# Performance work log

Measured on AMD Instinct MI355X. Metric: run time of the kernel, lower is better.

## Reference

```python
import jax, jax.numpy as jnp
import numpy as np

L, B, P, D, H, DH, KV, M, S, A = 12, 8, 800, 1024, 8, 256, 1, 4096, 50, 32
ROPE_BASE = 10000.0
NEG = -1e30


def _rms(x, w):
    return (x * jax.lax.rsqrt(jnp.mean(x * x, -1, keepdims=True) + 1e-6)) * (1.0 + w)


def _rope(x, cos, sin):
    # x: [B,h,S,DH]; cos/sin: [B,1,S,DH//2]
    x1, x2 = jnp.split(x, 2, axis=-1)
    return jnp.concatenate([x1 * cos - x2 * sin, x2 * cos + x1 * sin], -1)


def setup_inputs() -> dict:
    key = jax.random.key(0)
    ks = iter(jax.random.split(key, 40))
    def nrm(shape, s=0.02):
        return jax.random.normal(next(ks), shape, jnp.float32) * s
    return {
        'prefix_pad_masks': jnp.ones((B, P), jnp.bool_),
        'x_t': jax.random.normal(next(ks), (B, S, A), jnp.float32),
        'timestep': jax.random.uniform(next(ks), (B,), jnp.float32),
        'dt': jnp.full((1,), 0.1, jnp.float32),
        'cache_k': nrm((L, B, KV, P, DH), 1.0),
        'cache_v': nrm((L, B, KV, P, DH), 1.0),
        'w_act_in': nrm((A, D)), 'b_act_in': jnp.zeros((D,), jnp.float32),
        'w_t1': nrm((D, D)), 'b_t1': jnp.zeros((D,), jnp.float32),
        'w_t2': nrm((D, D)), 'b_t2': jnp.zeros((D,), jnp.float32),
        'ln1_w': jnp.zeros((L, D), jnp.float32),
        'ada1_w': nrm((L, D, D)),
        'ln2_w': jnp.zeros((L, D), jnp.float32),
        'wq': nrm((L, D, H * DH)), 'wk': nrm((L, D, KV * DH)),
        'wv': nrm((L, D, KV * DH)), 'wo': nrm((L, H * DH, D)),
        'wg': nrm((L, D, M)), 'wu': nrm((L, D, M)), 'wd': nrm((L, M, D)),
        'lnf_w': jnp.zeros((D,), jnp.float32), 'adaf_w': nrm((D, D)),
        'w_act_out': nrm((D, A)), 'b_act_out': jnp.zeros((A,), jnp.float32),
    }


def reference(prefix_pad_masks, x_t, timestep, dt, cache_k, cache_v,
              w_act_in, b_act_in, w_t1, b_t1, w_t2, b_t2,
              ln1_w, ada1_w, ln2_w, wq, wk, wv, wo, wg, wu, wd,
              lnf_w, adaf_w, w_act_out, b_act_out):
    b, s, _ = x_t.shape
    p = prefix_pad_masks.shape[1]
    # --- embed_suffix: action projection + sinusoidal time -> MLP -> adaRMS cond ---
    suffix = x_t @ w_act_in + b_act_in                              # [B,S,D]
    half = D // 2
    freqs = jnp.exp(-jnp.log(jnp.float32(10000.0)) * jnp.arange(half, dtype=jnp.float32) / half)
    ang = timestep[:, None] * freqs[None, :]
    temb = jnp.concatenate([jnp.sin(ang), jnp.cos(ang)], -1)        # [B,D]
    cond = jax.nn.silu(temb @ w_t1 + b_t1) @ w_t2 + b_t2            # adarms_cond [B,D]
    # --- prefix-suffix 2D attention mask (make_att_2d_masks_trt) ---
    suffix_pad = jnp.ones((b, s), jnp.int32)
    suffix_att = jnp.concatenate([jnp.ones((b, 1), jnp.int32), jnp.zeros((b, s - 1), jnp.int32)], 1)
    cums = jnp.cumsum(suffix_att, 1)
    att2d = cums[:, None, :] <= cums[:, :, None]
    pad2d = (suffix_pad[:, None, :] * suffix_pad[:, :, None]).astype(bool)
    pre2d = jnp.broadcast_to(prefix_pad_masks[:, None, :], (b, s, p))
    full = jnp.concatenate([pre2d, att2d & pad2d], 2)               # [B,S,P+S]
    bias = jnp.where(full, 0.0, NEG)[:, None, :, :].astype(jnp.float32)
    # --- position ids: prefix offset + suffix cumsum - 1 ---
    offs = jnp.sum(prefix_pad_masks.astype(jnp.int32), -1)[:, None]
    pos = offs + jnp.cumsum(suffix_pad, 1) - 1                      # [B,S]
    inv = 1.0 / (ROPE_BASE ** (jnp.arange(0, DH, 2, dtype=jnp.float32) / DH))
    rang = pos[..., None].astype(jnp.float32) * inv                 # [B,S,DH/2]
    cos = jnp.cos(rang)[:, None]
    sin = jnp.sin(rang)[:, None]
    # --- gemma expert (eager attention over KV cache + suffix) ---
    h = suffix * jnp.sqrt(jnp.float32(D))
    def layer(hc, xs):
        l1, a1, l2, Wq, Wk, Wv, Wo, Wg, Wu, Wd, ck, cv = xs
        x = _rms(hc, l1) * (1.0 + (cond @ a1)[:, None, :])
        q = (x @ Wq).reshape(b, s, H, DH).transpose(0, 2, 1, 3)
        k = (x @ Wk).reshape(b, s, KV, DH).transpose(0, 2, 1, 3)
        v = (x @ Wv).reshape(b, s, KV, DH).transpose(0, 2, 1, 3)
        q = _rope(q, cos, sin)
        k = _rope(k, cos, sin)
        kf = jnp.repeat(jnp.concatenate([ck, k], 2), H // KV, 1)    # [B,H,P+S,DH]
        vf = jnp.repeat(jnp.concatenate([cv, v], 2), H // KV, 1)
        sc = jnp.einsum('bhsd,bhtd->bhst', q, kf) / jnp.sqrt(jnp.float32(DH)) + bias
        at = jax.nn.softmax(sc, -1)
        o = jnp.einsum('bhst,bhtd->bhsd', at, vf).transpose(0, 2, 1, 3).reshape(b, s, H * DH)
        hc = hc + o @ Wo
        x2 = _rms(hc, l2)
        hc = hc + (jax.nn.gelu(x2 @ Wg, approximate=True) * (x2 @ Wu)) @ Wd
        return hc, None
    h, _ = jax.lax.scan(layer, h, (ln1_w, ada1_w, ln2_w, wq, wk, wv, wo, wg, wu, wd, cache_k, cache_v))
    hf = _rms(h, lnf_w) * (1.0 + (cond @ adaf_w)[:, None, :])
    v_t = hf[:, -S:].astype(jnp.float32) @ w_act_out + b_act_out    # action_out_proj
    return x_t + dt.reshape(1, 1, 1) * v_t                          # Euler step
```

## Files before the change

### kernel.cpp

```cpp
#include <hip/hip_runtime.h>
#include <hip/hip_bf16.h>
#include <math.h>

#define NLAYER 12
#define NB 8
#define NP 800
#define ND 1024
#define NH 8
#define NDH 256
#define NM 4096
#define NS 50
#define NA 32
#define NKEYS 850
#define KPAD 896

typedef unsigned short ushort_t;
typedef unsigned int u32;
using f32x4  = __attribute__((ext_vector_type(4))) float;
using short8 = __attribute__((ext_vector_type(8))) short;

__device__ __forceinline__ u32 pack_bf2(float lo, float hi) {
  u32 a = __float_as_uint(lo);
  u32 b = __float_as_uint(hi);
  a += 0x7fffu + ((a >> 16) & 1u);
  b += 0x7fffu + ((b >> 16) & 1u);
  return (a >> 16) | (b & 0xffff0000u);
}
__device__ __forceinline__ ushort_t bf1(float x) {
  u32 a = __float_as_uint(x);
  a += 0x7fffu + ((a >> 16) & 1u);
  return (ushort_t)(a >> 16);
}
__device__ __forceinline__ float ubf(ushort_t h) {
  return __uint_as_float(((u32)h) << 16);
}
__device__ __forceinline__ void async_cp16(const void* g, const void* l) {
  __builtin_amdgcn_global_load_lds(
      (const __attribute__((address_space(1))) u32*)g,
      (__attribute__((address_space(3))) u32*)l, 16, 0, 0);
}


__global__ void cvt_copy_kernel(const float* __restrict__ src, ushort_t* __restrict__ dst, long n) {
  long i = ((long)blockIdx.x * 256 + threadIdx.x) * 8;
  if (i >= n) return;
  const float4* s4 = reinterpret_cast<const float4*>(src + i);
  float4 a = s4[0], b = s4[1];
  *reinterpret_cast<uint4*>(dst + i) =
      make_uint4(pack_bf2(a.x, a.y), pack_bf2(a.z, a.w),
                 pack_bf2(b.x, b.y), pack_bf2(b.z, b.w));
}

template<int MODE>
__global__ __launch_bounds__(256) void transpose_cvt(
    const float* __restrict__ src, long sz, ushort_t* __restrict__ dst, long dz,
    int R, int C, int ldd, int halfOff) {
  __shared__ float Ls[64][65];
  const float* s = src + (long)blockIdx.z * sz;
  ushort_t* d    = dst + (long)blockIdx.z * dz;
  int c0 = blockIdx.x * 64, r0 = blockIdx.y * 64;
  int t = threadIdx.x;
  int rr = t >> 4;
  int cc = (t & 15) * 4;
#pragma unroll
  for (int j = 0; j < 4; ++j) {
    int rl = rr + j * 16;
    int r = r0 + rl;
    float4 v = make_float4(0.f, 0.f, 0.f, 0.f);
    if (r < R) v = *reinterpret_cast<const float4*>(s + (long)r * C + c0 + cc);
    Ls[rl][cc] = v.x; Ls[rl][cc+1] = v.y; Ls[rl][cc+2] = v.z; Ls[rl][cc+3] = v.w;
  }
  __syncthreads();
  int dr = t >> 2;
  int rc = (t & 3) * 16;
  int cg = c0 + dr;
  long orow;
  if (MODE == 0) orow = cg;
  else           orow = ((long)(cg >> 5) << 6) + (cg & 31) + halfOff;
  ushort_t* drow = d + orow * ldd + r0 + rc;
#pragma unroll
  for (int i = 0; i < 16; i += 2) {
    int sr = r0 + rc + i;
    if (sr < R) {
      u32 p = pack_bf2(Ls[rc + i][dr], Ls[rc + i + 1][dr]);
      *reinterpret_cast<u32*>(drow + i) = p;
    }
  }
}


__global__ void temb_kernel(const float* __restrict__ ts, float* __restrict__ temb) {
  int idx = blockIdx.x * 256 + threadIdx.x;
  if (idx >= NB * ND) return;
  int b = idx >> 10, d = idx & 1023;
  int i = d & 511;
  float f = __expf(-logf(10000.f) * (float)i / 512.f);
  float ang = ts[b] * f;
  temb[idx] = (d < 512) ? sinf(ang) : cosf(ang);
}

__global__ void suffix_kernel(const float* __restrict__ x_t, const float* __restrict__ w,
                              const float* __restrict__ bias, float* __restrict__ h) {
  int m = blockIdx.x;
  __shared__ float xs[NA];
  if (threadIdx.x < NA) xs[threadIdx.x] = x_t[m * NA + threadIdx.x];
  __syncthreads();
  for (int n = threadIdx.x; n < ND; n += 256) {
    float acc = bias[n];
#pragma unroll
    for (int k = 0; k < NA; ++k) acc += xs[k] * w[k * ND + n];
    h[m * ND + n] = acc * 32.0f;
  }
}

__global__ void rope_table_kernel(float* __restrict__ cosT, float* __restrict__ sinT) {
  int idx = blockIdx.x * 256 + threadIdx.x;
  if (idx >= NS * 128) return;
  int s = idx >> 7, i = idx & 127;
  float inv = __expf(-(float)(2 * i) / 256.f * logf(10000.f));
  float ang = (float)(NP + s) * inv;
  cosT[idx] = cosf(ang);
  sinT[idx] = sinf(ang);
}

__global__ void rope3_kernel(const ushort_t* __restrict__ qkv0, const ushort_t* __restrict__ qkv1,
                             const float* __restrict__ cosT, const float* __restrict__ sinT,
                             ushort_t* __restrict__ qT, ushort_t* __restrict__ k_new,
                             ushort_t* __restrict__ vT_l) {
  int idx = blockIdx.x * 256 + threadIdx.x;
  if (idx >= 400 * 10 * 128) return;
  int i = idx & 127;
  int rest = idx >> 7;
  int hh = rest % 10;
  int m = rest / 10;
  int b = m / NS, s = m % NS;
  if (hh == 9) {
    int d = i;
    long base = (long)m * 2560 + 2304;
    float v0 = ubf(qkv0[base + d])       + ubf(qkv1[base + d]);
    float v1 = ubf(qkv0[base + d + 128]) + ubf(qkv1[base + d + 128]);
    vT_l[((long)(b * 256 + d)) * KPAD + NP + s]       = bf1(v0);
    vT_l[((long)(b * 256 + d + 128)) * KPAD + NP + s] = bf1(v1);
    return;
  }
  float c = cosT[s * 128 + i], sn = sinT[s * 128 + i];
  if (hh < NH) {
    long base = (long)m * 2560 + hh * 256;
    float x1 = ubf(qkv0[base + i])       + ubf(qkv1[base + i]);
    float x2 = ubf(qkv0[base + 128 + i]) + ubf(qkv1[base + 128 + i]);
    ushort_t* dst = qT + (((long)(b * NH + hh) * NS + s) * 256);
    dst[i]       = bf1(x1 * c - x2 * sn);
    dst[128 + i] = bf1(x2 * c + x1 * sn);
  } else {
    long base = (long)m * 2560 + 2048;
    float x1 = ubf(qkv0[base + i])       + ubf(qkv1[base + i]);
    float x2 = ubf(qkv0[base + 128 + i]) + ubf(qkv1[base + 128 + i]);
    ushort_t* dst = k_new + (long)m * 256;
    dst[i]       = bf1(x1 * c - x2 * sn);
    dst[128 + i] = bf1(x2 * c + x1 * sn);
  }
}

template<bool BFOUT>
__global__ void rms_kernel(const float* __restrict__ hin, const float* __restrict__ w,
                           const float* __restrict__ ada, void* __restrict__ outv) {
  int m = blockIdx.x;
  int b = m / NS;
  int d0 = threadIdx.x * 4;
  float4 v = *reinterpret_cast<const float4*>(hin + (long)m * ND + d0);
  float ss = v.x*v.x + v.y*v.y + v.z*v.z + v.w*v.w;
#pragma unroll
  for (int off = 32; off > 0; off >>= 1) ss += __shfl_down(ss, off);
  __shared__ float red[4];
  int lane = threadIdx.x & 63, wid = threadIdx.x >> 6;
  if (lane == 0) red[wid] = ss;
  __syncthreads();
  float tot = red[0] + red[1] + red[2] + red[3];
  float r = rsqrtf(tot * (1.f / ND) + 1e-6f);
  float4 wv = *reinterpret_cast<const float4*>(w + d0);
  float4 o;
  o.x = v.x * r * (1.f + wv.x);
  o.y = v.y * r * (1.f + wv.y);
  o.z = v.z * r * (1.f + wv.z);
  o.w = v.w * r * (1.f + wv.w);
  if (ada) {
    float4 av = *reinterpret_cast<const float4*>(ada + (long)b * ND + d0);
    o.x *= (1.f + av.x); o.y *= (1.f + av.y); o.z *= (1.f + av.z); o.w *= (1.f + av.w);
  }
  if (BFOUT) {
    *reinterpret_cast<uint2*>((ushort_t*)outv + (long)m * ND + d0) =
        make_uint2(pack_bf2(o.x, o.y), pack_bf2(o.z, o.w));
  } else {
    *reinterpret_cast<float4*>((float*)outv + (long)m * ND + d0) = o;
  }
}

__global__ void softmax_kernel(const float* __restrict__ sc, ushort_t* __restrict__ P) {
  int row = blockIdx.x;
  const float* p = sc + (long)row * KPAD;
  ushort_t* o = P + (long)row * KPAD;
  __shared__ float e[NKEYS];
  __shared__ float red[4];
  int lane = threadIdx.x & 63, wid = threadIdx.x >> 6;
  float mx = -1e30f;
  for (int t = threadIdx.x; t < NKEYS; t += 256) { float v = p[t]; e[t] = v; mx = fmaxf(mx, v); }
#pragma unroll
  for (int off = 32; off > 0; off >>= 1) mx = fmaxf(mx, __shfl_down(mx, off));
  if (lane == 0) red[wid] = mx;
  __syncthreads();
  mx = fmaxf(fmaxf(red[0], red[1]), fmaxf(red[2], red[3]));
  __syncthreads();
  float sum = 0.f;
  for (int t = threadIdx.x; t < NKEYS; t += 256) {
    float v = __expf(e[t] - mx);
    e[t] = v;
    sum += v;
  }
#pragma unroll
  for (int off = 32; off > 0; off >>= 1) sum += __shfl_down(sum, off);
  if (lane == 0) red[wid] = sum;
  __syncthreads();
  float inv = 1.f / (red[0] + red[1] + red[2] + red[3]);
  for (int t = threadIdx.x; t < KPAD; t += 256)
    o[t] = (t < NKEYS) ? bf1(e[t] * inv) : (ushort_t)0;
}

__global__ void final_kernel(const float* __restrict__ hf, const float* __restrict__ w,
                             const float* __restrict__ bias, const float* __restrict__ x_t,
                             const float* __restrict__ dt, float* __restrict__ out) {
  int m = blockIdx.x;
  int a = threadIdx.x & 31;
  int kg = threadIdx.x >> 5;
  float acc = 0.f;
  for (int k = kg; k < ND; k += 8) acc += hf[(long)m * ND + k] * w[k * NA + a];
  __shared__ float red[256];
  red[threadIdx.x] = acc;
  __syncthreads();
  if (threadIdx.x < NA) {
    float s = 0.f;
#pragma unroll
    for (int g = 0; g < 8; ++g) s += red[g * 32 + a];
    out[m * NA + a] = x_t[m * NA + a] + dt[0] * (s + bias[a]);
  }
}

template<int EPI, bool SPL, bool SPLITK>
__global__ __launch_bounds__(256) void gemm64(
    const ushort_t* __restrict__ A, long az,
    const ushort_t* __restrict__ B1, long b1z,
    const ushort_t* __restrict__ B2, long b2z, int nsplit, int nlim2,
    void* __restrict__ Cv, long cz,
    int M, int N, int K, int lda, int ldb, int ldc,
    float scale, int kpb, const ushort_t* __restrict__ zpad) {
  int z = blockIdx.z;
  int chunk = 0;
  int kbeg = 0, kend = K;
  if (SPLITK) { chunk = z; kbeg = z * kpb; kend = kbeg + kpb; z = 0; }
  const ushort_t* Ab  = A  + (long)z * az;
  const ushort_t* B1b = B1 + (long)z * b1z;
  const ushort_t* B2b = SPL ? (B2 + (long)z * b2z) : nullptr;

  const int m0 = blockIdx.x * 64;
  const int n0 = blockIdx.y * 64;
  const int tid = threadIdx.x;
  const int lane = tid & 63;
  const int wbase = tid & 192;
  const int wid = wbase >> 6;
  const int wm = (wid >> 1) * 32;
  const int wn = (wid & 1) * 32;
  const int l15 = lane & 15;
  const int l4  = lane >> 4;

  __shared__ ushort_t As[2][64 * 64];
  __shared__ ushort_t Bs[2][64 * 64];

  f32x4 acc[2][2] = {};

  const int ci0 = wbase + lane;
  const int row0 = ci0 >> 3;
  const int kc0 = (ci0 & 7) << 3;
  const int ci1 = 256 + ci0;
  const int row1 = ci1 >> 3;
  const int kc1 = (ci1 & 7) << 3;
  int gra0 = m0 + row0; if (gra0 > M - 1) gra0 = M - 1;
  int gra1 = m0 + row1; if (gra1 > M - 1) gra1 = M - 1;
  const int n_0 = n0 + row0;
  const int n_1 = n0 + row1;

  auto stage = [&](int buf, int k0) {
    async_cp16(Ab + (long)gra0 * lda + k0 + kc0, (const char*)As[buf] + (wbase + lane) * 16 - lane * 16 + lane * 16);
    const ushort_t* gp0;
    const ushort_t* gp1;
    if (SPL) {
      gp0 = (n_0 < nsplit) ? B1b + (long)n_0 * ldb + k0 + kc0
          : (n_0 < nlim2)  ? B2b + (long)(n_0 - nsplit) * ldb + k0 + kc0
                           : zpad + kc0;
      gp1 = (n_1 < nsplit) ? B1b + (long)n_1 * ldb + k0 + kc1
          : (n_1 < nlim2)  ? B2b + (long)(n_1 - nsplit) * ldb + k0 + kc1
                           : zpad + kc1;
    } else {
      gp0 = B1b + (long)n_0 * ldb + k0 + kc0;
      gp1 = B1b + (long)n_1 * ldb + k0 + kc1;
    }
    async_cp16(gp0, (const char*)Bs[buf] + ci0 * 16);
    async_cp16(Ab + (long)gra1 * lda + k0 + kc1, (const char*)As[buf] + ci1 * 16);
    async_cp16(gp1, (const char*)Bs[buf] + ci1 * 16);
  };

  const int nt = (kend - kbeg) >> 6;
  stage(0, kbeg);
  __syncthreads();
  int cur = 0;
  for (int t = 0; t < nt; ++t) {
    if (t + 1 < nt) stage(cur ^ 1, kbeg + (t + 1) * 64);
    const ushort_t* Ac = As[cur];
    const ushort_t* Bc = Bs[cur];
#pragma unroll
    for (int ks = 0; ks < 2; ++ks) {
      short8 af[2], bf[2];
#pragma unroll
      for (int mi = 0; mi < 2; ++mi)
        af[mi] = *reinterpret_cast<const short8*>(&Ac[(wm + mi * 16 + l15) * 64 + ks * 32 + l4 * 8]);
#pragma unroll
      for (int ni = 0; ni < 2; ++ni)
        bf[ni] = *reinterpret_cast<const short8*>(&Bc[(wn + ni * 16 + l15) * 64 + ks * 32 + l4 * 8]);
#pragma unroll
      for (int mi = 0; mi < 2; ++mi)
#pragma unroll
        for (int ni = 0; ni < 2; ++ni)
          acc[mi][ni] = __builtin_amdgcn_mfma_f32_16x16x32_bf16(af[mi], bf[ni], acc[mi][ni], 0, 0, 0);
    }
    __syncthreads();
    cur ^= 1;
  }

#pragma unroll
  for (int mi = 0; mi < 2; ++mi) {
#pragma unroll
    for (int ni = 0; ni < 2; ++ni) {
      int col = n0 + wn + ni * 16 + l15;
      int rb  = m0 + wm + mi * 16 + l4 * 4;
      if (col >= N) continue;
#pragma unroll
      for (int r = 0; r < 4; ++r) {
        int row = rb + r;
        if (row >= M) continue;
        float v = acc[mi][ni][r];
        if (EPI == 0) {
          ((float*)Cv)[(long)z * cz + (long)row * ldc + col] = v * scale;
        } else if (EPI == 3) {
          atomicAdd(&((float*)Cv)[(long)row * ldc + col], v);
        } else if (EPI == 4) {
          int hh = row / NS;
          int s  = row - hh * NS;
          ((ushort_t*)Cv)[((long)(blockIdx.z * NS + s)) * 2048 + hh * 256 + col] = bf1(v);
        } else if (EPI == 5) {
          long slab = SPLITK ? (long)chunk : (long)z;
          ((ushort_t*)Cv)[slab * cz + (long)row * ldc + col] = bf1(v);
        }
      }
    }
  }
}

__global__ __launch_bounds__(256) void gemm64G(
    const ushort_t* __restrict__ A, const ushort_t* __restrict__ B,
    ushort_t* __restrict__ C, int M, int K, int lda, int ldb, int ldc) {
  const int m0 = blockIdx.x * 64;
  const int n0 = blockIdx.y * 64;
  const int tid = threadIdx.x;
  const int lane = tid & 63;
  const int wbase = tid & 192;
  const int wid = wbase >> 6;
  const int l15 = lane & 15;
  const int l4  = lane >> 4;

  __shared__ ushort_t As[2][64 * 64];
  __shared__ ushort_t Bs[2][64 * 64];

  f32x4 acc[4] = {};

  const int ci0 = wbase + lane;
  const int row0 = ci0 >> 3;
  const int kc0 = (ci0 & 7) << 3;
  const int ci1 = 256 + ci0;
  const int row1 = ci1 >> 3;
  const int kc1 = (ci1 & 7) << 3;
  int gra0 = m0 + row0; if (gra0 > M - 1) gra0 = M - 1;
  int gra1 = m0 + row1; if (gra1 > M - 1) gra1 = M - 1;

  auto stage = [&](int buf, int k0) {
    async_cp16(A + (long)gra0 * lda + k0 + kc0, (const char*)As[buf] + ci0 * 16);
    async_cp16(B + (long)(n0 + row0) * ldb + k0 + kc0, (const char*)Bs[buf] + ci0 * 16);
    async_cp16(A + (long)gra1 * lda + k0 + kc1, (const char*)As[buf] + ci1 * 16);
    async_cp16(B + (long)(n0 + row1) * ldb + k0 + kc1, (const char*)Bs[buf] + ci1 * 16);
  };

  const int nt = K >> 6;
  stage(0, 0);
  __syncthreads();
  int cur = 0;
  for (int t = 0; t < nt; ++t) {
    if (t + 1 < nt) stage(cur ^ 1, (t + 1) * 64);
    const ushort_t* Ac = As[cur];
    const ushort_t* Bc = Bs[cur];
#pragma unroll
    for (int ks = 0; ks < 2; ++ks) {
      short8 af = *reinterpret_cast<const short8*>(&Ac[(wid * 16 + l15) * 64 + ks * 32 + l4 * 8]);
#pragma unroll
      for (int ni = 0; ni < 4; ++ni) {
        short8 bf = *reinterpret_cast<const short8*>(&Bc[(ni * 16 + l15) * 64 + ks * 32 + l4 * 8]);
        acc[ni] = __builtin_amdgcn_mfma_f32_16x16x32_bf16(af, bf, acc[ni], 0, 0, 0);
      }
    }
    __syncthreads();
    cur ^= 1;
  }

#pragma unroll
  for (int ni = 0; ni < 2; ++ni) {
    int col = (n0 >> 1) + ni * 16 + l15;
    int rb  = m0 + wid * 16 + l4 * 4;
#pragma unroll
    for (int r = 0; r < 4; ++r) {
      int row = rb + r;
      if (row >= M) continue;
      float g = acc[ni][r];
      float u = acc[ni + 2][r];
      float inner = 0.7978845608028654f * (g + 0.044715f * g * g * g);
      float t = 0.5f * g * (1.f + tanhf(inner));
      C[(long)row * ldc + col] = bf1(t * u);
    }
  }
}

template<int EPI>
__global__ __launch_bounds__(256)
void gemm_f32_kernel(const float* __restrict__ A,
                     const float* __restrict__ B1,
                     float* __restrict__ C,
                     int M, int N, int K, int lda, int ldb, int ldc,
                     const float* __restrict__ bias) {
  const int m0 = blockIdx.x * 64;
  const int n0 = blockIdx.y * 64;
  const int tid = threadIdx.x;
  const int lane = tid & 63;
  const int wid = tid >> 6;
  const int wm = (wid >> 1) * 32;
  const int wn = (wid & 1) * 32;
  const int l15 = lane & 15;
  const int l4  = lane >> 4;

  __shared__ __align__(16) ushort_t As[64][72];
  __shared__ __align__(16) ushort_t Bs[64][72];

  f32x4 acc[2][2] = {};

  for (int k0 = 0; k0 < K; k0 += 64) {
#pragma unroll
    for (int pass = 0; pass < 2; ++pass) {
      int c = tid + pass * 256;
      int row = c >> 3;
      int kc = (c & 7) * 8;
      int gr = m0 + row, gk = k0 + kc;
      float v[8];
#pragma unroll
      for (int j = 0; j < 8; ++j)
        v[j] = (gr < M && gk + j < K) ? A[(long)gr * lda + gk + j] : 0.f;
      *reinterpret_cast<uint4*>(&As[row][kc]) =
          make_uint4(pack_bf2(v[0],v[1]), pack_bf2(v[2],v[3]),
                     pack_bf2(v[4],v[5]), pack_bf2(v[6],v[7]));
    }
    {
      int n = tid & 63;
      int kg = tid >> 6;
      int gn = n0 + n;
      u32 pk[8];
#pragma unroll
      for (int kk = 0; kk < 16; kk += 2) {
        int kga = k0 + kg * 16 + kk;
        float v0 = (gn < N && kga < K)     ? B1[(long)kga * ldb + gn] : 0.f;
        float v1 = (gn < N && kga + 1 < K) ? B1[(long)(kga + 1) * ldb + gn] : 0.f;
        pk[kk >> 1] = pack_bf2(v0, v1);
      }
      *reinterpret_cast<uint4*>(&Bs[n][kg * 16])     = make_uint4(pk[0],pk[1],pk[2],pk[3]);
      *reinterpret_cast<uint4*>(&Bs[n][kg * 16 + 8]) = make_uint4(pk[4],pk[5],pk[6],pk[7]);
    }
    __syncthreads();
#pragma unroll
    for (int ks = 0; ks < 2; ++ks) {
      short8 af[2], bfr[2];
#pragma unroll
      for (int mi = 0; mi < 2; ++mi)
        af[mi] = *reinterpret_cast<const short8*>(&As[wm + mi*16 + l15][ks*32 + l4*8]);
#pragma unroll
      for (int ni = 0; ni < 2; ++ni)
        bfr[ni] = *reinterpret_cast<const short8*>(&Bs[wn + ni*16 + l15][ks*32 + l4*8]);
#pragma unroll
      for (int mi = 0; mi < 2; ++mi)
#pragma unroll
        for (int ni = 0; ni < 2; ++ni)
          acc[mi][ni] = __builtin_amdgcn_mfma_f32_16x16x32_bf16(af[mi], bfr[ni], acc[mi][ni], 0, 0, 0);
    }
    __syncthreads();
  }

#pragma unroll
  for (int mi = 0; mi < 2; ++mi) {
#pragma unroll
    for (int ni = 0; ni < 2; ++ni) {
      int col = n0 + wn + ni * 16 + l15;
      int rb  = m0 + wm + mi * 16 + l4 * 4;
#pragma unroll
      for (int r = 0; r < 4; ++r) {
        int row = rb + r;
        if (row < M && col < N) {
          float v = acc[mi][ni][r];
          if (EPI == 1) C[(long)row * ldc + col] = v + bias[col];
          else {
            float t = v + bias[col];
            C[(long)row * ldc + col] = t / (1.f + __expf(-t));
          }
        }
      }
    }
  }
}

__global__ __launch_bounds__(256)
void gemm_f32sk(const float* __restrict__ A,
                const float* __restrict__ B, long bz,
                float* __restrict__ C, long cz,
                int M, int N, int K, int lda, int ldb, int ldc, int nks) {
  const int zz = blockIdx.z;
  const int layer = zz / nks;
  const int chunk = zz % nks;
  const int kpb = K / nks;
  const int kbeg = chunk * kpb, kend = kbeg + kpb;
  const float* Bb = B + (long)layer * bz;
  float* Cb = C + (long)layer * cz;

  const int m0 = blockIdx.x * 64;
  const int n0 = blockIdx.y * 64;
  const int tid = threadIdx.x;
  const int lane = tid & 63;
  const int wid = tid >> 6;
  const int wm = (wid >> 1) * 32;
  const int wn = (wid & 1) * 32;
  const int l15 = lane & 15;
  const int l4  = lane >> 4;

  __shared__ __align__(16) ushort_t As[64][72];
  __shared__ __align__(16) ushort_t Bs[64][72];

  f32x4 acc[2][2] = {};

  for (int k0 = kbeg; k0 < kend; k0 += 64) {
#pragma unroll
    for (int pass = 0; pass < 2; ++pass) {
      int c = tid + pass * 256;
      int row = c >> 3;
      int kc = (c & 7) * 8;
      int gr = m0 + row, gk = k0 + kc;
      float v[8];
#pragma unroll
      for (int j = 0; j < 8; ++j)
        v[j] = (gr < M) ? A[(long)gr * lda + gk + j] : 0.f;
      *reinterpret_cast<uint4*>(&As[row][kc]) =
          make_uint4(pack_bf2(v[0],v[1]), pack_bf2(v[2],v[3]),
                     pack_bf2(v[4],v[5]), pack_bf2(v[6],v[7]));
    }
    {
      int n = tid & 63;
      int kg = tid >> 6;
      int gn = n0 + n;
      u32 pk[8];
#pragma unroll
      for (int kk = 0; kk < 16; kk += 2) {
        int kga = k0 + kg * 16 + kk;
        float v0 = Bb[(long)kga * ldb + gn];
        float v1 = Bb[(long)(kga + 1) * ldb + gn];
        pk[kk >> 1] = pack_bf2(v0, v1);
      }
      *reinterpret_cast<uint4*>(&Bs[n][kg * 16])     = make_uint4(pk[0],pk[1],pk[2],pk[3]);
      *reinterpret_cast<uint4*>(&Bs[n][kg * 16 + 8]) = make_uint4(pk[4],pk[5],pk[6],pk[7]);
    }
    __syncthreads();
#pragma unroll
    for (int ks = 0; ks < 2; ++ks) {
      short8 af[2], bfr[2];
#pragma unroll
      for (int mi = 0; mi < 2; ++mi)
        af[mi] = *reinterpret_cast<const short8*>(&As[wm + mi*16 + l15][ks*32 + l4*8]);
#pragma unroll
      for (int ni = 0; ni < 2; ++ni)
        bfr[ni] = *reinterpret_cast<const short8*>(&Bs[wn + ni*16 + l15][ks*32 + l4*8]);
#pragma unroll
      for (int mi = 0; mi < 2; ++mi)
#pragma unroll
        for (int ni = 0; ni < 2; ++ni)
          acc[mi][ni] = __builtin_amdgcn_mfma_f32_16x16x32_bf16(af[mi], bfr[ni], acc[mi][ni], 0, 0, 0);
    }
    __syncthreads();
  }

#pragma unroll
  for (int mi = 0; mi < 2; ++mi) {
#pragma unroll
    for (int ni = 0; ni < 2; ++ni) {
      int col = n0 + wn + ni * 16 + l15;
      int rb  = m0 + wm + mi * 16 + l4 * 4;
#pragma unroll
      for (int r = 0; r < 4; ++r) {
        int row = rb + r;
        if (row < M && col < N)
          atomicAdd(&Cb[(long)row * ldc + col], acc[mi][ni][r]);
      }
    }
  }
}

extern "C" void kernel_launch(void* const* d_in, const int* in_sizes, int n_in,
                              void* d_out, int out_size, void* d_ws, size_t ws_size,
                              hipStream_t stream) {
  (void)in_sizes; (void)n_in; (void)out_size; (void)ws_size;
  const float* x_t      = (const float*)d_in[1];
  const float* tstep    = (const float*)d_in[2];
  const float* dtp      = (const float*)d_in[3];
  const float* cache_k  = (const float*)d_in[4];
  const float* cache_v  = (const float*)d_in[5];
  const float* w_act_in = (const float*)d_in[6];
  const float* b_act_in = (const float*)d_in[7];
  const float* w_t1     = (const float*)d_in[8];
  const float* b_t1     = (const float*)d_in[9];
  const float* w_t2     = (const float*)d_in[10];
  const float* b_t2     = (const float*)d_in[11];
  const float* ln1_w    = (const float*)d_in[12];
  const float* ada1_w   = (const float*)d_in[13];
  const float* ln2_w    = (const float*)d_in[14];
  const float* wq       = (const float*)d_in[15];
  const float* wk       = (const float*)d_in[16];
  const float* wv       = (const float*)d_in[17];
  const float* wo       = (const float*)d_in[18];
  const float* wg       = (const float*)d_in[19];
  const float* wu       = (const float*)d_in[20];
  const float* wd       = (const float*)d_in[21];
  const float* lnf_w    = (const float*)d_in[22];
  const float* adaf_w   = (const float*)d_in[23];
  const float* wao      = (const float*)d_in[24];
  const float* bao      = (const float*)d_in[25];
  float* outp = (float*)d_out;

  char* p = (char*)d_ws;
  auto alloc = [&](size_t bytes) { char* r = p; p += (bytes + 255) & ~(size_t)255; return r; };

  ushort_t* wqkvT  = (ushort_t*)alloc((size_t)12 * 2560 * 1024 * 2);
  ushort_t* woT    = (ushort_t*)alloc((size_t)12 * 1024 * 2048 * 2);
  ushort_t* wguT   = (ushort_t*)alloc((size_t)12 * 8192 * 1024 * 2);
  ushort_t* wdT    = (ushort_t*)alloc((size_t)12 * 1024 * 4096 * 2);
  ushort_t* kcache = (ushort_t*)alloc((size_t)12 * 8 * NP * 256 * 2);
  ushort_t* vT     = (ushort_t*)alloc((size_t)12 * 8 * 256 * KPAD * 2);
  ushort_t* qkvp   = (ushort_t*)alloc((size_t)2 * 400 * 2560 * 2);
  ushort_t* qT     = (ushort_t*)alloc((size_t)8 * 400 * 256 * 2);
  ushort_t* k_new  = (ushort_t*)alloc((size_t)400 * 256 * 2);
  float*    sc     = (float*)alloc((size_t)8 * 400 * KPAD * 4);
  ushort_t* P      = (ushort_t*)alloc((size_t)8 * 400 * KPAD * 2);
  ushort_t* o_buf  = (ushort_t*)alloc((size_t)400 * 2048 * 2);
  ushort_t* t_buf  = (ushort_t*)alloc((size_t)400 * 4096 * 2);
  ushort_t* x_buf  = (ushort_t*)alloc((size_t)400 * 1024 * 2);
  float*    h_buf  = (float*)alloc((size_t)400 * 1024 * 4);
  float*    hf     = (float*)alloc((size_t)400 * 1024 * 4);
  float*    temb   = (float*)alloc(8 * 1024 * 4);
  float*    tmp    = (float*)alloc(8 * 1024 * 4);
  float*    cond   = (float*)alloc(8 * 1024 * 4);
  float*    ada_all= (float*)alloc((size_t)12 * 8 * 1024 * 4);
  float*    adaf_o = (float*)alloc(8 * 1024 * 4);
  float*    cosT   = (float*)alloc(NS * 128 * 4);
  float*    sinT   = (float*)alloc(NS * 128 * 4);
  ushort_t* zpad   = (ushort_t*)alloc(512 * 2);

  hipMemsetAsync(zpad, 0, 512 * 2, stream);
  hipMemsetAsync(ada_all, 0, ((size_t)12 * 8 * 1024 + 8 * 1024) * 4, stream);

  {
    long n = (long)12 * 8 * NP * 256;
    cvt_copy_kernel<<<(int)((n / 8 + 255) / 256), 256, 0, stream>>>(cache_k, kcache, n);
  }
  transpose_cvt<0><<<dim3(32, 16, 12), 256, 0, stream>>>(wq, (long)1024 * 2048, wqkvT, (long)2560 * 1024, 1024, 2048, 1024, 0);
  transpose_cvt<0><<<dim3(4, 16, 12), 256, 0, stream>>>(wk, (long)1024 * 256, wqkvT + (long)2048 * 1024, (long)2560 * 1024, 1024, 256, 1024, 0);
  transpose_cvt<0><<<dim3(4, 16, 12), 256, 0, stream>>>(wv, (long)1024 * 256, wqkvT + (long)2304 * 1024, (long)2560 * 1024, 1024, 256, 1024, 0);
  transpose_cvt<0><<<dim3(16, 32, 12), 256, 0, stream>>>(wo, (long)2048 * 1024, woT, (long)1024 * 2048, 2048, 1024, 2048, 0);
  transpose_cvt<1><<<dim3(64, 16, 12), 256, 0, stream>>>(wg, (long)1024 * 4096, wguT, (long)8192 * 1024, 1024, 4096, 1024, 0);
  transpose_cvt<1><<<dim3(64, 16, 12), 256, 0, stream>>>(wu, (long)1024 * 4096, wguT, (long)8192 * 1024, 1024, 4096, 1024, 32);
  transpose_cvt<0><<<dim3(16, 64, 12), 256, 0, stream>>>(wd, (long)4096 * 1024, wdT, (long)1024 * 4096, 4096, 1024, 4096, 0);
  transpose_cvt<0><<<dim3(4, 13, 96), 256, 0, stream>>>(cache_v, (long)NP * 256, vT, (long)256 * KPAD, NP, 256, KPAD, 0);

  temb_kernel<<<32, 256, 0, stream>>>(tstep, temb);
  suffix_kernel<<<400, 256, 0, stream>>>(x_t, w_act_in, b_act_in, h_buf);
  rope_table_kernel<<<25, 256, 0, stream>>>(cosT, sinT);
  gemm_f32_kernel<2><<<dim3(1, 16, 1), 256, 0, stream>>>(temb, w_t1, tmp, NB, ND, ND, ND, ND, ND, b_t1);
  gemm_f32_kernel<1><<<dim3(1, 16, 1), 256, 0, stream>>>(tmp, w_t2, cond, NB, ND, ND, ND, ND, ND, b_t2);
  gemm_f32sk<<<dim3(1, 16, 48), 256, 0, stream>>>(cond, ada1_w, (long)ND * ND, ada_all, (long)NB * ND, NB, ND, ND, ND, ND, ND, 4);
  gemm_f32sk<<<dim3(1, 16, 4), 256, 0, stream>>>(cond, adaf_w, 0, adaf_o, 0, NB, ND, ND, ND, ND, ND, 4);

  for (int l = 0; l < NLAYER; ++l) {
    rms_kernel<true><<<400, 256, 0, stream>>>(h_buf, ln1_w + (long)l * ND, ada_all + (long)l * NB * ND, x_buf);
    gemm64<5, false, true><<<dim3(7, 40, 2), 256, 0, stream>>>(
        x_buf, 0, wqkvT + (long)l * 2560 * 1024, 0, nullptr, 0, 0, 0,
        qkvp, (long)400 * 2560, 400, 2560, 1024, 1024, 1024, 2560, 1.f, 512, zpad);
    rope3_kernel<<<2000, 256, 0, stream>>>(qkvp, qkvp + (long)400 * 2560, cosT, sinT,
                                           qT, k_new, vT + (long)l * 8 * 256 * KPAD);
    gemm64<0, true, false><<<dim3(7, 14, 8), 256, 0, stream>>>(
        qT, (long)400 * 256,
        kcache + (long)l * 8 * NP * 256, (long)NP * 256,
        k_new, (long)NS * 256, NP, NKEYS,
        sc, (long)400 * KPAD, 400, KPAD, 256, 256, 256, KPAD, 0.0625f, 0, zpad);
    softmax_kernel<<<3200, 256, 0, stream>>>(sc, P);
    gemm64<4, false, false><<<dim3(7, 4, 8), 256, 0, stream>>>(
        P, (long)400 * KPAD,
        vT + (long)l * 8 * 256 * KPAD, (long)256 * KPAD, nullptr, 0, 0, 0,
        o_buf, 0, 400, 256, KPAD, KPAD, KPAD, 2048, 1.f, 0, zpad);
    gemm64<3, false, true><<<dim3(7, 16, 4), 256, 0, stream>>>(
        o_buf, 0, woT + (long)l * 1024 * 2048, 0, nullptr, 0, 0, 0,
        h_buf, 0, 400, 1024, 2048, 2048, 2048, 1024, 1.f, 512, zpad);
    rms_kernel<true><<<400, 256, 0, stream>>>(h_buf, ln2_w + (long)l * ND, nullptr, x_buf);
    gemm64G<<<dim3(7, 128, 1), 256, 0, stream>>>(
        x_buf, wguT + (long)l * 8192 * 1024, t_buf, 400, 1024, 1024, 1024, 4096);
    gemm64<3, false, true><<<dim3(7, 16, 4), 256, 0, stream>>>(
        t_buf, 0, wdT + (long)l * 1024 * 4096, 0, nullptr, 0, 0, 0,
        h_buf, 0, 400, 1024, 4096, 4096, 4096, 1024, 1.f, 1024, zpad);
  }

  rms_kernel<false><<<400, 256, 0, stream>>>(h_buf, lnf_w, adaf_o, hf);
  final_kernel<<<400, 256, 0, stream>>>(hf, wao, bao, x_t, dtp, outp);
}
```

Measured before the change: 2.049 ms.

## Use 128x128 block tiles for QKV, gate-up, and down projections

Adds a 128x128-tile MFMA GEMM kernel in which each wave computes a 64x64 sub-tile, and uses it for the QKV projection, the fused gate/up GELU projection and the down projection, replacing the 64x64 kernels. Larger tiles raise operand reuse from shared memory and global memory for each MFMA, which cuts load traffic. The cost is fewer blocks (for example 4x20x2 and 4x8x8), more LDS and registers per block, and lower occupancy. The down projection also moves to 8-way split-K with atomic adds, which doubles the atomic traffic into h_buf. With M=400, the last row tile of 128 is mostly padding.

```diff
diff --git a/kernel.cpp b/kernel.cpp
--- a/kernel.cpp
+++ b/kernel.cpp
@@ -288,7 +288,7 @@
   const int n_1 = n0 + row1;
 
   auto stage = [&](int buf, int k0) {
-    async_cp16(Ab + (long)gra0 * lda + k0 + kc0, (const char*)As[buf] + (wbase + lane) * 16 - lane * 16 + lane * 16);
+    async_cp16(Ab + (long)gra0 * lda + k0 + kc0, (const char*)As[buf] + ci0 * 16);
     const ushort_t* gp0;
     const ushort_t* gp1;
     if (SPL) {
@@ -363,37 +363,135 @@
   }
 }
 
-__global__ __launch_bounds__(256) void gemm64G(
+template<int EPI, bool SPLITK>
+__global__ __launch_bounds__(256) void gemm128(
+    const ushort_t* __restrict__ A,
+    const ushort_t* __restrict__ B,
+    void* __restrict__ Cv, long cz,
+    int M, int K, int lda, int ldb, int ldc, int kpb) {
+  const int chunk = SPLITK ? blockIdx.z : 0;
+  const int kbeg = SPLITK ? chunk * kpb : 0;
+  const int kend = SPLITK ? kbeg + kpb : K;
+
+  const int m0 = blockIdx.x * 128;
+  const int n0 = blockIdx.y * 128;
+  const int tid = threadIdx.x;
+  const int lane = tid & 63;
+  const int wid = tid >> 6;
+  const int wm = (wid >> 1) * 64;
+  const int wn = (wid & 1) * 64;
+  const int l15 = lane & 15;
+  const int l4  = lane >> 4;
+
+  __shared__ ushort_t As[2][128 * 64];
+  __shared__ ushort_t Bs[2][128 * 64];
+
+  f32x4 acc[4][4] = {};
+
+  int arow[4], brow[4], kcs[4];
+#pragma unroll
+  for (int i = 0; i < 4; ++i) {
+    int ci = i * 256 + tid;
+    int row = ci >> 3;
+    kcs[i] = (ci & 7) << 3;
+    int gr = m0 + row; if (gr > M - 1) gr = M - 1;
+    arow[i] = gr;
+    brow[i] = n0 + row;
+  }
+
+  auto stage = [&](int buf, int k0) {
+#pragma unroll
+    for (int i = 0; i < 4; ++i) {
+      int ci = i * 256 + tid;
+      async_cp16(A + (long)arow[i] * lda + k0 + kcs[i], (const char*)As[buf] + ci * 16);
+      async_cp16(B + (long)brow[i] * ldb + k0 + kcs[i], (const char*)Bs[buf] + ci * 16);
+    }
+  };
+
+  const int nt = (kend - kbeg) >> 6;
+  stage(0, kbeg);
+  __syncthreads();
+  int cur = 0;
+  for (int t = 0; t < nt; ++t) {
+    if (t + 1 < nt) stage(cur ^ 1, kbeg + (t + 1) * 64);
+    const ushort_t* Ac = As[cur];
+    const ushort_t* Bc = Bs[cur];
+#pragma unroll
+    for (int ks = 0; ks < 2; ++ks) {
+      short8 af[4], bf[4];
+#pragma unroll
+      for (int mi = 0; mi < 4; ++mi)
+        af[mi] = *reinterpret_cast<const short8*>(&Ac[(wm + mi * 16 + l15) * 64 + ks * 32 + l4 * 8]);
+#pragma unroll
+      for (int ni = 0; ni < 4; ++ni)
+        bf[ni] = *reinterpret_cast<const short8*>(&Bc[(wn + ni * 16 + l15) * 64 + ks * 32 + l4 * 8]);
+#pragma unroll
+      for (int mi = 0; mi < 4; ++mi)
+#pragma unroll
+        for (int ni = 0; ni < 4; ++ni)
+          acc[mi][ni] = __builtin_amdgcn_mfma_f32_16x16x32_bf16(af[mi], bf[ni], acc[mi][ni], 0, 0, 0);
+    }
+    __syncthreads();
+    cur ^= 1;
+  }
+
+#pragma unroll
+  for (int mi = 0; mi < 4; ++mi) {
+#pragma unroll
+    for (int ni = 0; ni < 4; ++ni) {
+      int col = n0 + wn + ni * 16 + l15;
+      int rb  = m0 + wm + mi * 16 + l4 * 4;
+#pragma unroll
+      for (int r = 0; r < 4; ++r) {
+        int row = rb + r;
+        if (row >= M) continue;
+        float v = acc[mi][ni][r];
+        if (EPI == 3) {
+          atomicAdd(&((float*)Cv)[(long)row * ldc + col], v);
+        } else {
+          ((ushort_t*)Cv)[(long)chunk * cz + (long)row * ldc + col] = bf1(v);
+        }
+      }
+    }
+  }
+}
+
+__global__ __launch_bounds__(256) void gemm128G(
     const ushort_t* __restrict__ A, const ushort_t* __restrict__ B,
     ushort_t* __restrict__ C, int M, int K, int lda, int ldb, int ldc) {
-  const int m0 = blockIdx.x * 64;
-  const int n0 = blockIdx.y * 64;
+  const int m0 = blockIdx.x * 128;
+  const int n0 = blockIdx.y * 128;
   const int tid = threadIdx.x;
   const int lane = tid & 63;
-  const int wbase = tid & 192;
-  const int wid = wbase >> 6;
+  const int wid = tid >> 6;
+  const int wm = (wid >> 1) * 64;
+  const int wn = (wid & 1) * 64;
   const int l15 = lane & 15;
   const int l4  = lane >> 4;
 
-  __shared__ ushort_t As[2][64 * 64];
-  __shared__ ushort_t Bs[2][64 * 64];
-
-  f32x4 acc[4] = {};
-
-  const int ci0 = wbase + lane;
-  const int row0 = ci0 >> 3;
-  const int kc0 = (ci0 & 7) << 3;
-  const int ci1 = 256 + ci0;
-  const int row1 = ci1 >> 3;
-  const int kc1 = (ci1 & 7) << 3;
-  int gra0 = m0 + row0; if (gra0 > M - 1) gra0 = M - 1;
-  int gra1 = m0 + row1; if (gra1 > M - 1) gra1 = M - 1;
+  __shared__ ushort_t As[2][128 * 64];
+  __shared__ ushort_t Bs[2][128 * 64];
+
+  f32x4 acc[4][4] = {};
+
+  int arow[4], brow[4], kcs[4];
+#pragma unroll
+  for (int i = 0; i < 4; ++i) {
+    int ci = i * 256 + tid;
+    int row = ci >> 3;
+    kcs[i] = (ci & 7) << 3;
+    int gr = m0 + row; if (gr > M - 1) gr = M - 1;
+    arow[i] = gr;
+    brow[i] = n0 + row;
+  }
 
   auto stage = [&](int buf, int k0) {
-    async_cp16(A + (long)gra0 * lda + k0 + kc0, (const char*)As[buf] + ci0 * 16);
-    async_cp16(B + (long)(n0 + row0) * ldb + k0 + kc0, (const char*)Bs[buf] + ci0 * 16);
-    async_cp16(A + (long)gra1 * lda + k0 + kc1, (const char*)As[buf] + ci1 * 16);
-    async_cp16(B + (long)(n0 + row1) * ldb + k0 + kc1, (const char*)Bs[buf] + ci1 * 16);
+#pragma unroll
+    for (int i = 0; i < 4; ++i) {
+      int ci = i * 256 + tid;
+      async_cp16(A + (long)arow[i] * lda + k0 + kcs[i], (const char*)As[buf] + ci * 16);
+      async_cp16(B + (long)brow[i] * ldb + k0 + kcs[i], (const char*)Bs[buf] + ci * 16);
+    }
   };
 
   const int nt = K >> 6;
@@ -406,30 +504,40 @@
     const ushort_t* Bc = Bs[cur];
 #pragma unroll
     for (int ks = 0; ks < 2; ++ks) {
-      short8 af = *reinterpret_cast<const short8*>(&Ac[(wid * 16 + l15) * 64 + ks * 32 + l4 * 8]);
-#pragma unroll
-      for (int ni = 0; ni < 4; ++ni) {
-        short8 bf = *reinterpret_cast<const short8*>(&Bc[(ni * 16 + l15) * 64 + ks * 32 + l4 * 8]);
-        acc[ni] = __builtin_amdgcn_mfma_f32_16x16x32_bf16(af, bf, acc[ni], 0, 0, 0);
-      }
+      short8 af[4], bf[4];
+#pragma unroll
+      for (int mi = 0; mi < 4; ++mi)
+        af[mi] = *reinterpret_cast<const short8*>(&Ac[(wm + mi * 16 + l15) * 64 + ks * 32 + l4 * 8]);
+#pragma unroll
+      for (int ni = 0; ni < 4; ++ni)
+        bf[ni] = *reinterpret_cast<const short8*>(&Bc[(wn + ni * 16 + l15) * 64 + ks * 32 + l4 * 8]);
+#pragma unroll
+      for (int mi = 0; mi < 4; ++mi)
+#pragma unroll
+        for (int ni = 0; ni < 4; ++ni)
+          acc[mi][ni] = __builtin_amdgcn_mfma_f32_16x16x32_bf16(af[mi], bf[ni], acc[mi][ni], 0, 0, 0);
     }
     __syncthreads();
     cur ^= 1;
   }
 
-#pragma unroll
-  for (int ni = 0; ni < 2; ++ni) {
-    int col = (n0 >> 1) + ni * 16 + l15;
-    int rb  = m0 + wid * 16 + l4 * 4;
-#pragma unroll
-    for (int r = 0; r < 4; ++r) {
-      int row = rb + r;
-      if (row >= M) continue;
-      float g = acc[ni][r];
-      float u = acc[ni + 2][r];
-      float inner = 0.7978845608028654f * (g + 0.044715f * g * g * g);
-      float t = 0.5f * g * (1.f + tanhf(inner));
-      C[(long)row * ldc + col] = bf1(t * u);
+  const int gI = (n0 + wn) >> 6;
+#pragma unroll
+  for (int mi = 0; mi < 4; ++mi) {
+#pragma unroll
+    for (int ni = 0; ni < 2; ++ni) {
+      int col = gI * 32 + ni * 16 + l15;
+      int rb  = m0 + wm + mi * 16 + l4 * 4;
+#pragma unroll
+      for (int r = 0; r < 4; ++r) {
+        int row = rb + r;
+        if (row >= M) continue;
+        float g = acc[mi][ni][r];
+        float u = acc[mi][ni + 2][r];
+        float inner = 0.7978845608028654f * (g + 0.044715f * g * g * g);
+        float t = 0.5f * g * (1.f + tanhf(inner));
+        C[(long)row * ldc + col] = bf1(t * u);
+      }
     }
   }
 }
@@ -705,9 +813,9 @@
 
   for (int l = 0; l < NLAYER; ++l) {
     rms_kernel<true><<<400, 256, 0, stream>>>(h_buf, ln1_w + (long)l * ND, ada_all + (long)l * NB * ND, x_buf);
-    gemm64<5, false, true><<<dim3(7, 40, 2), 256, 0, stream>>>(
-        x_buf, 0, wqkvT + (long)l * 2560 * 1024, 0, nullptr, 0, 0, 0,
-        qkvp, (long)400 * 2560, 400, 2560, 1024, 1024, 1024, 2560, 1.f, 512, zpad);
+    gemm128<5, true><<<dim3(4, 20, 2), 256, 0, stream>>>(
+        x_buf, wqkvT + (long)l * 2560 * 1024,
+        qkvp, (long)400 * 2560, 400, 1024, 1024, 1024, 2560, 512);
     rope3_kernel<<<2000, 256, 0, stream>>>(qkvp, qkvp + (long)400 * 2560, cosT, sinT,
                                            qT, k_new, vT + (long)l * 8 * 256 * KPAD);
     gemm64<0, true, false><<<dim3(7, 14, 8), 256, 0, stream>>>(
@@ -724,11 +832,11 @@
         o_buf, 0, woT + (long)l * 1024 * 2048, 0, nullptr, 0, 0, 0,
         h_buf, 0, 400, 1024, 2048, 2048, 2048, 1024, 1.f, 512, zpad);
     rms_kernel<true><<<400, 256, 0, stream>>>(h_buf, ln2_w + (long)l * ND, nullptr, x_buf);
-    gemm64G<<<dim3(7, 128, 1), 256, 0, stream>>>(
+    gemm128G<<<dim3(4, 64, 1), 256, 0, stream>>>(
         x_buf, wguT + (long)l * 8192 * 1024, t_buf, 400, 1024, 1024, 1024, 4096);
-    gemm64<3, false, true><<<dim3(7, 16, 4), 256, 0, stream>>>(
-        t_buf, 0, wdT + (long)l * 1024 * 4096, 0, nullptr, 0, 0, 0,
-        h_buf, 0, 400, 1024, 4096, 4096, 4096, 1024, 1.f, 1024, zpad);
+    gemm128<3, true><<<dim3(4, 8, 8), 256, 0, stream>>>(
+        t_buf, wdT + (long)l * 1024 * 4096,
+        h_buf, 0, 400, 4096, 4096, 4096, 1024, 512);
   }
 
   rms_kernel<false><<<400, 256, 0, stream>>>(h_buf, lnf_w, adaf_o, hf);
```

After: 2.163 ms. +5.6%, slower.
